# Optimization experiments

Hardware: AMD Instinct MI355X
Metric: run time of the kernel (lower is better)

## Reference

```python
import jax, jax.numpy as jnp
import numpy as np

DIM = 512
NUM_STEPS = 1000
MIN_OMEGA = 0.1
MAX_OMEGA = 10.1
DT = 0.001
INPUT_SCALER = 5.0
BETA1 = 1.0


def setup_inputs() -> dict:
    key = jax.random.key(0)
    k1, k2, k3 = jax.random.split(key, 3)
    B, T, D = 32, NUM_STEPS, DIM
    X_r = jax.random.normal(k1, (B, T, D), dtype=jnp.float32)
    X_i = jax.random.normal(k2, (B, T, D), dtype=jnp.float32)
    # layer parameter: omega_init ~ U(-1, 1), shape (1, dim)
    omegas = jax.random.uniform(k3, (1, D), minval=-1.0, maxval=1.0, dtype=jnp.float32)
    return {"X_r": X_r, "X_i": X_i, "omegas": omegas}


def _hopf(X_r, X_i, omegas):
    # omega mapping: scale to [min, max] Hz then to rad/s
    omega = (omegas * (MAX_OMEGA - MIN_OMEGA) + MIN_OMEGA) * (2.0 * np.pi)  # [1, D]
    B, T, D = X_r.shape
    r0 = jnp.ones((B, D), dtype=X_r.dtype)
    phi0 = jnp.zeros((B, D), dtype=X_r.dtype)

    def step(carry, xs):
        r_t, phis = carry
        xr, xi = xs  # each [B, D]
        input_r = INPUT_SCALER * xr * jnp.cos(phis)
        input_phi = INPUT_SCALER * xi * jnp.sin(phis)
        r_t = r_t + ((1.0 - BETA1 * jnp.square(r_t)) * r_t + input_r) * DT
        phis = phis + (omega - input_phi) * DT
        return (r_t, phis), (r_t, phis)

    xs = (jnp.swapaxes(X_r, 0, 1), jnp.swapaxes(X_i, 0, 1))  # [T, B, D]
    _, (r_seq, phi_seq) = jax.lax.scan(step, (r0, phi0), xs)
    r = jnp.swapaxes(r_seq, 0, 1)    # [B, T, D]
    phi = jnp.swapaxes(phi_seq, 0, 1)
    z_real = r * jnp.cos(phi)
    z_imag = r * jnp.sin(phi)
    return z_real, z_imag


def reference(X_r, X_i, omegas):
    return _hopf(X_r, X_i, omegas)
```

## Files before the change

kernel.cpp:

```cpp
#include <hip/hip_runtime.h>
#include <hip/hip_bf16.h>


#define B 32
#define T 1000
#define D 512
#define DTc 0.001f
#define K_IN 0.005f
#define KREV 7.95774715e-4f
#define U 20
#define NB (T / U)
#define NOPS (U / 4)
#define RING 5

typedef float v4f __attribute__((ext_vector_type(4)));
typedef const __attribute__((address_space(1))) float gfloat;
typedef __attribute__((address_space(3))) float lfloat;

#define SCHEDB() __builtin_amdgcn_sched_barrier(0)
#define BAR()    __builtin_amdgcn_s_barrier()
#define W_LGKM0  0xC07F
#define W_VM30   0x4F7E
#define W_VM40   0x8F78
#define W_VM50   0xCF72
#define W_VM60   0xCF7C

__global__ __launch_bounds__(128, 1) void hopf_scan(
    const float* __restrict__ Xr, const float* __restrict__ Xi,
    const float* __restrict__ om,
    float* __restrict__ zr, float* __restrict__ zi) {
    const int tid = threadIdx.x;
    const int bb = blockIdx.x;
    const int b = bb >> 3;
    const int dblk = (bb & 7) << 6;
    const size_t blkoff = (size_t)b * (T * D) + dblk;

    __shared__ __align__(16) float INr[RING][U][64];
    __shared__ __align__(16) float INi[RING][U][64];
    __shared__ __align__(16) float OUTr[2][U][64];
    __shared__ __align__(16) float OUTi[2][U][64];

    if (tid < 64) {
        const int i = tid;
        const float od = __builtin_fmaf(om[dblk + i], 10.0f, 0.1f) * DTc;
        float r = 1.0f, phi = 0.0f, c = 1.0f, s = 0.0f;

        BAR();
        int ib = 0;
        for (int n = 0; n < NB; ++n) {
            const int ob = n & 1;

            float xr[U], xi[U];
#pragma unroll
            for (int t = 0; t < U; ++t) {
                xr[t] = INr[ib][t][i];
                xi[t] = INi[ib][t][i];
            }
            SCHEDB();

#pragma unroll
            for (int t = 0; t < U; ++t) {
                const float omr2 = __builtin_fmaf(-r, r, 1.0f);
                r = __builtin_fmaf(omr2 * r, DTc, r);
                r = __builtin_fmaf(K_IN * xr[t], c, r);
                phi = __builtin_fmaf(-(KREV * xi[t]), s, phi + od);
                s = __builtin_amdgcn_sinf(phi);
                c = __builtin_amdgcn_cosf(phi);
                OUTr[ob][t][i] = r * c;
                OUTi[ob][t][i] = r * s;
            }
            __builtin_amdgcn_s_waitcnt(W_LGKM0);
            SCHEDB();
            BAR();
            ib = (ib == RING - 1) ? 0 : ib + 1;
        }
    } else {
        const int i = tid - 64;
        const int ts = i >> 4;
        const int dq = (i & 15) << 2;
        const float* __restrict__ xr_blk = Xr + blkoff;
        const float* __restrict__ xi_blk = Xi + blkoff;
        float* __restrict__ zr_blk = zr + blkoff;
        float* __restrict__ zi_blk = zi + blkoff;

        auto issueglds = [&](int body, int buf) {
#pragma unroll
            for (int k = 0; k < NOPS; ++k) {
                const size_t off = (size_t)(body * U + 4 * k + ts) * D + dq;
                __builtin_amdgcn_global_load_lds((gfloat*)(xr_blk + off),
                                                 (lfloat*)&INr[buf][4 * k][0], 16, 0, 0);
                __builtin_amdgcn_global_load_lds((gfloat*)(xi_blk + off),
                                                 (lfloat*)&INi[buf][4 * k][0], 16, 0, 0);
            }
        };
        auto drainbody = [&](int body) {
            const int ob = body & 1;
#pragma unroll
            for (int k = 0; k < NOPS; ++k) {
                const size_t off = (size_t)(body * U + 4 * k + ts) * D + dq;
                const v4f vr = *reinterpret_cast<const v4f*>(&OUTr[ob][4 * k + ts][dq]);
                const v4f vi = *reinterpret_cast<const v4f*>(&OUTi[ob][4 * k + ts][dq]);
                __builtin_nontemporal_store(vr, reinterpret_cast<v4f*>(zr_blk + off));
                __builtin_nontemporal_store(vi, reinterpret_cast<v4f*>(zi_blk + off));
            }
        };

        issueglds(0, 0);
        issueglds(1, 1);
        issueglds(2, 2);
        issueglds(3, 3);
        __builtin_amdgcn_s_waitcnt(W_VM30);
        SCHEDB();
        BAR();

        int bufn = 4;
        for (int n = 0; n < NB; ++n) {
            if (n + 4 < NB) issueglds(n + 4, bufn);
            SCHEDB();
            if (n + 1 < NB) {
                const int after = 10 * ((n + 2 < NB) + (n + 3 < NB) + (n + 4 < NB))
                                + 10 * ((n >= 2) + (n >= 3) + (n >= 4));
                if (after >= 60)      __builtin_amdgcn_s_waitcnt(W_VM60);
                else if (after == 50) __builtin_amdgcn_s_waitcnt(W_VM50);
                else if (after == 40) __builtin_amdgcn_s_waitcnt(W_VM40);
                else                  __builtin_amdgcn_s_waitcnt(W_VM30);
            }
            SCHEDB();
            if (n >= 1) drainbody(n - 1);
            SCHEDB();
            BAR();
            bufn = (bufn == RING - 1) ? 0 : bufn + 1;
        }
        drainbody(NB - 1);
    }
}

extern "C" void kernel_launch(void* const* d_in, const int* in_sizes, int n_in,
                              void* d_out, int out_size, void* d_ws, size_t ws_size,
                              hipStream_t stream) {
    const float* Xr = (const float*)d_in[0];
    const float* Xi = (const float*)d_in[1];
    const float* om = (const float*)d_in[2];
    float* zr = (float*)d_out;
    float* zi = zr + (size_t)B * T * D;

    hopf_scan<<<dim3(B * D / 64), dim3(128), 0, stream>>>(Xr, Xi, om, zr, zi);
}
```

Measured before the change: 45.59 us.

## Store outputs directly from compute wave instead of staging through LDS

The compute wave now writes each step's z_real/z_imag straight to global memory with scalar nontemporal stores, coalesced across the 64 lanes. This removes the LDS output buffers, the LDS write wait, and the loader wave's drain of vectorized stores. The loader wave's vmcnt wait thresholds are recomputed because it no longer issues stores. The trade-off is that store issue now lands on the latency-critical serial compute wave, and it uses 4-byte rather than 16-byte stores.

Result: slower. 48.91 us (+7.3%).

```diff
diff --git a/kernel.cpp b/kernel.cpp
--- a/kernel.cpp
+++ b/kernel.cpp
@@ -13,17 +13,15 @@
 #define NOPS (U / 4)
 #define RING 5
 
-typedef float v4f __attribute__((ext_vector_type(4)));
 typedef const __attribute__((address_space(1))) float gfloat;
 typedef __attribute__((address_space(3))) float lfloat;
 
 #define SCHEDB() __builtin_amdgcn_sched_barrier(0)
 #define BAR()    __builtin_amdgcn_s_barrier()
-#define W_LGKM0  0xC07F
 #define W_VM30   0x4F7E
-#define W_VM40   0x8F78
-#define W_VM50   0xCF72
-#define W_VM60   0xCF7C
+#define W_VM20   0x4F74
+#define W_VM10   0x0F7A
+#define W_VM0    0x0F70
 
 __global__ __launch_bounds__(128, 1) void hopf_scan(
     const float* __restrict__ Xr, const float* __restrict__ Xi,
@@ -37,19 +35,18 @@
 
     __shared__ __align__(16) float INr[RING][U][64];
     __shared__ __align__(16) float INi[RING][U][64];
-    __shared__ __align__(16) float OUTr[2][U][64];
-    __shared__ __align__(16) float OUTi[2][U][64];
 
     if (tid < 64) {
         const int i = tid;
         const float od = __builtin_fmaf(om[dblk + i], 10.0f, 0.1f) * DTc;
         float r = 1.0f, phi = 0.0f, c = 1.0f, s = 0.0f;
 
+        float* __restrict__ zr_p = zr + blkoff + i;
+        float* __restrict__ zi_p = zi + blkoff + i;
+
         BAR();
         int ib = 0;
         for (int n = 0; n < NB; ++n) {
-            const int ob = n & 1;
-
             float xr[U], xi[U];
 #pragma unroll
             for (int t = 0; t < U; ++t) {
@@ -66,10 +63,11 @@
                 phi = __builtin_fmaf(-(KREV * xi[t]), s, phi + od);
                 s = __builtin_amdgcn_sinf(phi);
                 c = __builtin_amdgcn_cosf(phi);
-                OUTr[ob][t][i] = r * c;
-                OUTi[ob][t][i] = r * s;
+                __builtin_nontemporal_store(r * c, zr_p);
+                __builtin_nontemporal_store(r * s, zi_p);
+                zr_p += D;
+                zi_p += D;
             }
-            __builtin_amdgcn_s_waitcnt(W_LGKM0);
             SCHEDB();
             BAR();
             ib = (ib == RING - 1) ? 0 : ib + 1;
@@ -80,8 +78,6 @@
         const int dq = (i & 15) << 2;
         const float* __restrict__ xr_blk = Xr + blkoff;
         const float* __restrict__ xi_blk = Xi + blkoff;
-        float* __restrict__ zr_blk = zr + blkoff;
-        float* __restrict__ zi_blk = zi + blkoff;
 
         auto issueglds = [&](int body, int buf) {
 #pragma unroll
@@ -91,17 +87,6 @@
                                                  (lfloat*)&INr[buf][4 * k][0], 16, 0, 0);
                 __builtin_amdgcn_global_load_lds((gfloat*)(xi_blk + off),
                                                  (lfloat*)&INi[buf][4 * k][0], 16, 0, 0);
-            }
-        };
-        auto drainbody = [&](int body) {
-            const int ob = body & 1;
-#pragma unroll
-            for (int k = 0; k < NOPS; ++k) {
-                const size_t off = (size_t)(body * U + 4 * k + ts) * D + dq;
-                const v4f vr = *reinterpret_cast<const v4f*>(&OUTr[ob][4 * k + ts][dq]);
-                const v4f vi = *reinterpret_cast<const v4f*>(&OUTi[ob][4 * k + ts][dq]);
-                __builtin_nontemporal_store(vr, reinterpret_cast<v4f*>(zr_blk + off));
-                __builtin_nontemporal_store(vi, reinterpret_cast<v4f*>(zi_blk + off));
             }
         };
 
@@ -118,20 +103,16 @@
             if (n + 4 < NB) issueglds(n + 4, bufn);
             SCHEDB();
             if (n + 1 < NB) {
-                const int after = 10 * ((n + 2 < NB) + (n + 3 < NB) + (n + 4 < NB))
-                                + 10 * ((n >= 2) + (n >= 3) + (n >= 4));
-                if (after >= 60)      __builtin_amdgcn_s_waitcnt(W_VM60);
-                else if (after == 50) __builtin_amdgcn_s_waitcnt(W_VM50);
-                else if (after == 40) __builtin_amdgcn_s_waitcnt(W_VM40);
-                else                  __builtin_amdgcn_s_waitcnt(W_VM30);
+                const int after = 10 * ((n + 2 < NB) + (n + 3 < NB) + (n + 4 < NB));
+                if (after == 30)      __builtin_amdgcn_s_waitcnt(W_VM30);
+                else if (after == 20) __builtin_amdgcn_s_waitcnt(W_VM20);
+                else if (after == 10) __builtin_amdgcn_s_waitcnt(W_VM10);
+                else                  __builtin_amdgcn_s_waitcnt(W_VM0);
             }
-            SCHEDB();
-            if (n >= 1) drainbody(n - 1);
             SCHEDB();
             BAR();
             bufn = (bufn == RING - 1) ? 0 : bufn + 1;
         }
-        drainbody(NB - 1);
     }
 }
 
```
